# Kernel optimization log

Hardware: AMD Instinct MI355X
Metric: run time of the kernel (lower is better)

The kernel has to match this reference:

```python
import jax, jax.numpy as jnp
import numpy as np

B, S, D, H = 4, 1024, 256, 8  # batch, seq, d_model (== head_dim), n_heads
SCALE = 1.0 / float(np.sqrt(D))  # source references undefined self.scale; use 1/sqrt(d_model)


def setup_inputs() -> dict:
    key = jax.random.key(0)
    ks = jax.random.split(key, 11)
    w = 0.02
    return {
        "value_input": jax.random.normal(ks[0], (B, S, D), dtype=jnp.float32),
        "key_input": jax.random.normal(ks[1], (B, S, D), dtype=jnp.float32),
        "query_input": jax.random.normal(ks[2], (B, S, D), dtype=jnp.float32),
        "Wv": jax.random.normal(ks[3], (D, D * H), dtype=jnp.float32) * w,
        "bv": jnp.zeros((D * H,), dtype=jnp.float32),
        "Wk": jax.random.normal(ks[4], (D, D * H), dtype=jnp.float32) * w,
        "bk": jnp.zeros((D * H,), dtype=jnp.float32),
        "Wq": jax.random.normal(ks[5], (D, D * H), dtype=jnp.float32) * w,
        "bq": jnp.zeros((D * H,), dtype=jnp.float32),
        "Wo": jax.random.normal(ks[6], (D * H, D), dtype=jnp.float32) * w,
        "bo": jnp.zeros((D,), dtype=jnp.float32),
    }


def reference(value_input, key_input, query_input, Wv, bv, Wk, bk, Wq, bq, Wo, bo):
    # Fused QKV-style projections, then split into heads along last dim.
    # torch.split(..., d_model, dim=-1) == reshape to (B, S, H, D).
    v = (value_input @ Wv + bv).reshape(B, S, H, D)
    k = (key_input @ Wk + bk).reshape(B, S, H, D)
    q = (query_input @ Wq + bq).reshape(B, S, H, D)
    # Source: dot = k @ q^T  -> scores[b,h,key_pos,query_pos]
    scores = jnp.einsum('bkhd,bqhd->bhkq', k, q) * SCALE
    # Softmax over dim=-1 == the QUERY axis (faithful to source, nonstandard).
    attn = jax.nn.softmax(scores, axis=-1)
    # attn @ v : contract query axis with v's seq axis -> output indexed by key pos
    out_h = jnp.einsum('bhkq,bqhd->bkhd', attn, v)
    concat = out_h.reshape(B, S, H * D)
    return concat @ Wo + bo
```

## Files before the change

### kernel.cpp

```cpp
#include <hip/hip_runtime.h>
#include <cstddef>
#include <cstdint>

#define Bz 4
#define Sz 1024
#define Dm 256
#define Hh 8
#define DHh 2048
#define SCALE 0.0625f

typedef __attribute__((ext_vector_type(8))) short short8;
typedef __attribute__((ext_vector_type(16))) float f32x16;

__device__ inline unsigned short f2bf(float f){
  unsigned u = __float_as_uint(f);
  u += 0x7FFFu + ((u >> 16) & 1u);
  return (unsigned short)(u >> 16);
}
__device__ inline unsigned pk2(float a, float b){
  return (unsigned)f2bf(a) | ((unsigned)f2bf(b) << 16);
}
__device__ inline void gll16(const void* g, void* l){
  __builtin_amdgcn_global_load_lds((const __attribute__((address_space(1))) unsigned*)g,
                                   (__attribute__((address_space(3))) unsigned*)l, 16, 0, 0);
}
__device__ inline short8 lds8(const char* p){ return *(const short8*)p; }
__device__ inline f32x16 MM(short8 a, short8 b, f32x16 c){
  return __builtin_amdgcn_mfma_f32_32x32x16_bf16(a, b, c, 0, 0, 0);
}
__device__ inline f32x16 z16(){ f32x16 v;
#pragma unroll
  for(int i=0;i<16;i++) v[i]=0.f; return v; }

__global__ __launch_bounds__(256) void cvt_all(
    const float* __restrict__ S0, const float* __restrict__ S1, const float* __restrict__ S2,
    unsigned short* __restrict__ D0, unsigned short* __restrict__ D1, unsigned short* __restrict__ D2,
    const float* __restrict__ W0, const float* __restrict__ W1,
    const float* __restrict__ W2, const float* __restrict__ W3,
    unsigned short* __restrict__ T0, unsigned short* __restrict__ T1,
    unsigned short* __restrict__ T2, unsigned short* __restrict__ T3){
  __shared__ float t[32][33];
  int bx = blockIdx.x;
  if(bx < 3072){
    const int seg = bx >> 10;
    const float* src = seg==0 ? S0 : seg==1 ? S1 : S2;
    unsigned short* dst = seg==0 ? D0 : seg==1 ? D1 : D2;
    const int i = (bx & 1023)*256 + threadIdx.x;
    float4 v = ((const float4*)src)[i];
    ushort4 o; o.x=f2bf(v.x); o.y=f2bf(v.y); o.z=f2bf(v.z); o.w=f2bf(v.w);
    ((ushort4*)dst)[i] = o;
    return;
  }
  bx -= 3072;
  const int z = bx >> 9, inner = bx & 511;
  const float* W = z==0 ? W0 : z==1 ? W1 : z==2 ? W2 : W3;
  unsigned short* T = z==0 ? T0 : z==1 ? T1 : z==2 ? T2 : T3;
  const int K = (z<3) ? 256 : 2048;
  const int N = (z<3) ? 2048 : 256;
  const int n0 = (z<3) ? (inner & 63)*32 : (inner & 7)*32;
  const int k0 = (z<3) ? (inner >> 6)*32 : (inner >> 3)*32;
  const int a = threadIdx.x >> 5, c = threadIdx.x & 31;
#pragma unroll
  for(int p=0;p<4;p++)
    t[a + p*8][c] = W[(size_t)(k0 + a + p*8)*N + n0 + c];
  __syncthreads();
#pragma unroll
  for(int p=0;p<4;p++)
    T[(size_t)(n0 + a + p*8)*K + k0 + c] = f2bf(t[c][a + p*8]);
}

__global__ __launch_bounds__(256) void gemm_proj_all(
    const unsigned short* __restrict__ A0, const unsigned short* __restrict__ A1,
    const unsigned short* __restrict__ A2,
    const unsigned short* __restrict__ B0, const unsigned short* __restrict__ B1,
    const unsigned short* __restrict__ B2,
    const float* __restrict__ bias0, const float* __restrict__ bias1,
    const float* __restrict__ bias2,
    unsigned short* __restrict__ C0, unsigned short* __restrict__ C1,
    unsigned short* __restrict__ C2){
  __shared__ __align__(16) char sm[65536];
  const int z = blockIdx.z;
  const unsigned short* A = z==0 ? A0 : z==1 ? A1 : A2;
  const unsigned short* Bt = z==0 ? B0 : z==1 ? B1 : B2;
  const float* bias = z==0 ? bias0 : z==1 ? bias1 : bias2;
  unsigned short* C = z==0 ? C0 : z==1 ? C1 : C2;
  const int tid = threadIdx.x, w = tid>>6, lane = tid&63, l31 = lane&31, hp = lane>>5;
  const int wm = (w>>1)*64, wn = (w&1)*64;
  const int bm = blockIdx.y*128, bn = blockIdx.x*128;
  f32x16 acc[2][2]; acc[0][0]=z16(); acc[0][1]=z16(); acc[1][0]=z16(); acc[1][1]=z16();

  auto STAGE = [&](int db, int kk){
#pragma unroll
    for(int j=0;j<4;j++){
      int ci = (w*4+j)*64 + lane;
      int m = ci>>3, sl = ci&7;
      gll16(A  + (size_t)(bm+m)*256 + kk + ((sl ^ (m&7))<<3), sm + db*32768 + (w*4+j)*1024);
      gll16(Bt + (size_t)(bn+m)*256 + kk + ((sl ^ (m&7))<<3), sm + db*32768 + 16384 + (w*4+j)*1024);
    }
  };

  STAGE(0, 0);
  __syncthreads();
  int db = 0;
  for(int t=0; t<4; ++t){
    if(t<3) STAGE(db^1, (t+1)*64);
    const char* base = sm + db*32768;
#pragma unroll
    for(int s=0;s<4;s++){
      int m0 = wm + l31, m1 = wm + 32 + l31;
      int n0 = wn + l31, n1 = wn + 32 + l31;
      short8 a0 = lds8(base + m0*128 + (((s*2+hp) ^ (m0&7))<<4));
      short8 a1 = lds8(base + m1*128 + (((s*2+hp) ^ (m1&7))<<4));
      short8 b0 = lds8(base + 16384 + n0*128 + (((s*2+hp) ^ (n0&7))<<4));
      short8 b1 = lds8(base + 16384 + n1*128 + (((s*2+hp) ^ (n1&7))<<4));
      acc[0][0] = MM(a0,b0,acc[0][0]); acc[0][1] = MM(a0,b1,acc[0][1]);
      acc[1][0] = MM(a1,b0,acc[1][0]); acc[1][1] = MM(a1,b1,acc[1][1]);
    }
    __syncthreads();
    db ^= 1;
  }
#pragma unroll
  for(int nh=0; nh<2; nh++){
    int ncol = bn + wn + nh*32 + l31;
    float bb = bias[ncol];
#pragma unroll
    for(int mh=0; mh<2; mh++){
      if(z == 0){
        int hidx = ncol >> 8, d = ncol & 255;
#pragma unroll
        for(int gq=0; gq<4; gq++){
          int mrow = bm + wm + mh*32 + 8*gq + 4*hp;
          int batch = mrow >> 10, sin = mrow & 1023;
          unsigned u0 = pk2(acc[mh][nh][4*gq+0] + bb, acc[mh][nh][4*gq+1] + bb);
          unsigned u1 = pk2(acc[mh][nh][4*gq+2] + bb, acc[mh][nh][4*gq+3] + bb);
          uint2 uu; uu.x = u0; uu.y = u1;
          *(uint2*)(C + ((size_t)((batch*Hh + hidx)*Dm + d))*Sz + sin) = uu;
        }
      } else {
        float sc = (z == 1) ? SCALE : 1.0f;
#pragma unroll
        for(int r=0; r<16; r++){
          int mrow = bm + wm + mh*32 + (r&3) + 8*(r>>2) + 4*hp;
          C[(size_t)mrow*DHh + ncol] = f2bf((acc[mh][nh][r] + bb) * sc);
        }
      }
    }
  }
}

__global__ __launch_bounds__(256, 2) void attn_mfma(
    const unsigned short* __restrict__ Kp, const unsigned short* __restrict__ Qp,
    const unsigned short* __restrict__ Vt, unsigned short* __restrict__ Oc){
  __shared__ __align__(16) char sm[66560];
  const int tid = threadIdx.x, w = tid>>6, lane = tid&63, l31 = lane&31, hp = lane>>5;
  const int rg = w&1, set = w>>1;
  const int bid = blockIdx.x;
  const int xcd = bid & 7, inner = bid >> 3;
  const int rb = inner & 15, gsub = inner >> 4;
  const int g = gsub*8 + xcd, b = g >> 3, h = g & 7;
  const int brow0 = rb * 64;
  const size_t vtbase = ((size_t)((b*Hh + h)*Dm))*Sz;

  short8 kp[16];
  {
    const unsigned short* kr = Kp + (size_t)(b*Sz + brow0 + rg*32 + l31)*DHh + h*Dm + hp*8;
#pragma unroll
    for(int ki=0; ki<16; ki++) kp[ki] = *(const short8*)(kr + ki*16);
  }
  f32x16 acc[8];
#pragma unroll
  for(int f=0; f<8; f++) acc[f] = z16();
  float m_run = -3.0e38f, l_run = 0.f;
  char* qpL = sm + set*16384;
  char* vtL = sm + 32768 + set*16384;

  auto STAGE = [&](int it){
    const int kv0 = set*512 + it*32;
#pragma unroll
    for(int j=0; j<8; j++){
      int slot = j*2 + rg;
      int ci = slot*64 + lane;
      int c = ci>>5, sl5 = ci&31;
      gll16(Qp + (size_t)(b*Sz + kv0 + c)*DHh + h*Dm + ((sl5 ^ c)<<3),
            qpL + slot*1024);
      int dp = ci>>3, sv = (ci&7) ^ (dp&7);
      int d = dp*2 + (sv>>2), co = (sv&3)*8;
      gll16(Vt + vtbase + (size_t)d*Sz + kv0 + co, vtL + slot*1024);
    }
  };

  STAGE(0);
  __syncthreads();
  for(int it=0; it<16; ++it){
    f32x16 S = z16();
#pragma unroll
    for(int ki=0; ki<16; ki++){
      short8 a = lds8(qpL + l31*512 + (((ki*2+hp) ^ l31)<<4));
      S = MM(a, kp[ki], S);
    }
    float tmax = S[0];
#pragma unroll
    for(int r=1; r<16; r++) tmax = fmaxf(tmax, S[r]);
    tmax = fmaxf(tmax, __shfl_xor(tmax, 32));
    if(!__all(tmax <= m_run + 8.0f)){
      float mnew = fmaxf(m_run, tmax);
      float alpha = __expf(m_run - mnew);
      m_run = mnew; l_run *= alpha;
#pragma unroll
      for(int r=0; r<16; r++){
        int rr = (r&3) + 8*(r>>2) + 4*hp;
        float ar = __shfl(alpha, rr);
#pragma unroll
        for(int f=0; f<8; f++) acc[f][r] *= ar;
      }
    }
    float lsum = 0.f;
#pragma unroll
    for(int r=0; r<16; r++){ S[r] = __expf(S[r] - m_run); lsum += S[r]; }
    lsum += __shfl_xor(lsum, 32);
    l_run += lsum;
    short8 pa[2];
#pragma unroll
    for(int t=0; t<2; t++){
      unsigned w01 = pk2(S[t*8+0], S[t*8+1]);
      unsigned w23 = pk2(S[t*8+2], S[t*8+3]);
      unsigned w45 = pk2(S[t*8+4], S[t*8+5]);
      unsigned w67 = pk2(S[t*8+6], S[t*8+7]);
      unsigned x01 = __shfl_xor(w01, 32), x23 = __shfl_xor(w23, 32);
      unsigned x45 = __shfl_xor(w45, 32), x67 = __shfl_xor(w67, 32);
      union { unsigned u[4]; short8 s8; } U;
      if(hp == 0){ U.u[0]=w01; U.u[1]=w23; U.u[2]=x01; U.u[3]=x23; }
      else       { U.u[0]=x45; U.u[1]=x67; U.u[2]=w45; U.u[3]=w67; }
      pa[t] = U.s8;
    }
#pragma unroll
    for(int t=0; t<2; t++){
#pragma unroll
      for(int f=0; f<8; f++){
        int d = f*32 + l31;
        int dp = d>>1;
        int slot = (d&1)*4 + t*2 + hp;
        short8 vfr = lds8(vtL + dp*128 + ((slot ^ (dp&7))<<4));
        acc[f] = MM(pa[t], vfr, acc[f]);
      }
    }
    if(it < 15){
      __syncthreads();
      STAGE(it+1);
      __syncthreads();
    }
  }
  __syncthreads();
  float* stats = (float*)(sm + 65536);
  if(lane < 32){ stats[(w*32 + lane)*2 + 0] = m_run; stats[(w*32 + lane)*2 + 1] = l_run; }
  __syncthreads();
  float* mg = (float*)sm + rg*8192;
  if(set == 1){
    float mA = stats[(rg*32 + l31)*2 + 0];
    float mf = fmaxf(mA, m_run);
    float bB = __expf(m_run - mf);
#pragma unroll
    for(int r=0; r<16; r++){
      int rr = (r&3) + 8*(r>>2) + 4*hp;
      float br = __shfl(bB, rr);
#pragma unroll
      for(int f=0; f<8; f++) mg[rr*256 + f*32 + l31] = acc[f][r]*br;
    }
  }
  __syncthreads();
  if(set == 0){
    float mB = stats[((2+rg)*32 + l31)*2 + 0];
    float lB = stats[((2+rg)*32 + l31)*2 + 1];
    float mf = fmaxf(m_run, mB);
    float bA = __expf(m_run - mf), bBv = __expf(mB - mf);
    float inv = 1.0f / (l_run*bA + lB*bBv);
#pragma unroll
    for(int r=0; r<16; r++){
      int rr = (r&3) + 8*(r>>2) + 4*hp;
      float bAr = __shfl(bA, rr);
      float invr = __shfl(inv, rr);
      int srow = brow0 + rg*32 + rr;
#pragma unroll
      for(int f=0; f<8; f++){
        float v = (acc[f][r]*bAr + mg[rr*256 + f*32 + l31]) * invr;
        Oc[(size_t)(b*Sz + srow)*DHh + h*Dm + f*32 + l31] = f2bf(v);
      }
    }
  }
}

__global__ __launch_bounds__(256) void gemm_out(const unsigned short* __restrict__ A,
    const unsigned short* __restrict__ Bt, const float* __restrict__ bias,
    float* __restrict__ C){
  __shared__ __align__(16) char sm[32768];
  const int tid = threadIdx.x, w = tid>>6, lane = tid&63, l31 = lane&31, hp = lane>>5;
  const int wm = (w>>1)*32, wn = (w&1)*32;
  const int bm = blockIdx.y*64, bn = blockIdx.x*64;
  f32x16 acc = z16();

  auto STAGE = [&](int db, int kk){
#pragma unroll
    for(int j=0; j<2; j++){
      int ci = (w*2+j)*64 + lane;
      int m = ci>>3, sl = ci&7;
      gll16(A  + (size_t)(bm+m)*DHh + kk + ((sl ^ (m&7))<<3), sm + db*16384 + (w*2+j)*1024);
      gll16(Bt + (size_t)(bn+m)*DHh + kk + ((sl ^ (m&7))<<3), sm + db*16384 + 8192 + (w*2+j)*1024);
    }
  };

  STAGE(0, 0);
  __syncthreads();
  int db = 0;
  for(int t=0; t<32; ++t){
    if(t<31) STAGE(db^1, (t+1)*64);
    const char* base = sm + db*16384;
#pragma unroll
    for(int s=0; s<4; s++){
      int m0 = wm + l31, n0 = wn + l31;
      short8 a = lds8(base + m0*128 + (((s*2+hp) ^ (m0&7))<<4));
      short8 b = lds8(base + 8192 + n0*128 + (((s*2+hp) ^ (n0&7))<<4));
      acc = MM(a, b, acc);
    }
    __syncthreads();
    db ^= 1;
  }
  float bb = bias[bn + wn + l31];
#pragma unroll
  for(int r=0; r<16; r++){
    int mrow = bm + wm + (r&3) + 8*(r>>2) + 4*hp;
    C[(size_t)mrow*Dm + bn + wn + l31] = acc[r] + bb;
  }
}

extern "C" void kernel_launch(void* const* d_in, const int* in_sizes, int n_in,
                              void* d_out, int out_size, void* d_ws, size_t ws_size,
                              hipStream_t stream){
  (void)in_sizes; (void)n_in; (void)out_size; (void)ws_size;
  const float* value_in = (const float*)d_in[0];
  const float* key_in   = (const float*)d_in[1];
  const float* query_in = (const float*)d_in[2];
  const float* Wv = (const float*)d_in[3];
  const float* bv = (const float*)d_in[4];
  const float* Wk = (const float*)d_in[5];
  const float* bk = (const float*)d_in[6];
  const float* Wq = (const float*)d_in[7];
  const float* bq = (const float*)d_in[8];
  const float* Wo = (const float*)d_in[9];
  const float* bo = (const float*)d_in[10];

  char* ws = (char*)d_ws;
  unsigned short* av  = (unsigned short*)(ws + ((size_t) 0u<<20));
  unsigned short* ak  = (unsigned short*)(ws + ((size_t) 2u<<20));
  unsigned short* aq  = (unsigned short*)(ws + ((size_t) 4u<<20));
  unsigned short* wtv = (unsigned short*)(ws + ((size_t) 6u<<20));
  unsigned short* wtk = (unsigned short*)(ws + ((size_t) 7u<<20));
  unsigned short* wtq = (unsigned short*)(ws + ((size_t) 8u<<20));
  unsigned short* wto = (unsigned short*)(ws + ((size_t) 9u<<20));
  unsigned short* vt  = (unsigned short*)(ws + ((size_t)10u<<20));
  unsigned short* kb  = (unsigned short*)(ws + ((size_t)26u<<20));
  unsigned short* qb  = (unsigned short*)(ws + ((size_t)42u<<20));
  unsigned short* cc  = (unsigned short*)(ws + ((size_t)58u<<20));

  cvt_all<<<5120, 256, 0, stream>>>(value_in, key_in, query_in, av, ak, aq,
                                    Wv, Wk, Wq, Wo, wtv, wtk, wtq, wto);

  gemm_proj_all<<<dim3(16, 32, 3), 256, 0, stream>>>(
      av, ak, aq, wtv, wtk, wtq, bv, bk, bq, vt, kb, qb);

  attn_mfma<<<512, 256, 0, stream>>>(kb, qb, vt, cc);

  gemm_out<<<dim3(4, 64), 256, 0, stream>>>(cc, wto, bo, (float*)d_out);
}
```

Before: 253.3 us.

## Restructure attention: 512-thread blocks, double-buffered Q, V read from global in fragment layout

The V projection output is written in a blocked layout (seq blocks of 8 × d × 8), so the attention kernel can load V fragments straight from global memory into registers instead of staging them through LDS. Only Q is staged, now double-buffered so the next tile's load overlaps the current compute, which removes one barrier per iteration. Blocks grow to 512 threads covering 128 rows with a new block-to-head mapping, and MFMA sections are wrapped in s_setprio. The cost is more global-load traffic and latency on V, plus higher register pressure under the new launch bounds.

```diff
diff --git a/kernel.cpp b/kernel.cpp
--- a/kernel.cpp
+++ b/kernel.cpp
@@ -131,10 +131,11 @@
         for(int gq=0; gq<4; gq++){
           int mrow = bm + wm + mh*32 + 8*gq + 4*hp;
           int batch = mrow >> 10, sin = mrow & 1023;
+          int sblk = sin >> 3;
           unsigned u0 = pk2(acc[mh][nh][4*gq+0] + bb, acc[mh][nh][4*gq+1] + bb);
           unsigned u1 = pk2(acc[mh][nh][4*gq+2] + bb, acc[mh][nh][4*gq+3] + bb);
           uint2 uu; uu.x = u0; uu.y = u1;
-          *(uint2*)(C + ((size_t)((batch*Hh + hidx)*Dm + d))*Sz + sin) = uu;
+          *(uint2*)(C + ((size_t)((batch*Hh + hidx)*128 + sblk)*256 + d)*8 + 4*hp) = uu;
         }
       } else {
         float sc = (z == 1) ? SCALE : 1.0f;
@@ -148,22 +149,21 @@
   }
 }
 
-__global__ __launch_bounds__(256, 2) void attn_mfma(
+__global__ __launch_bounds__(512, 2) void attn_mfma(
     const unsigned short* __restrict__ Kp, const unsigned short* __restrict__ Qp,
     const unsigned short* __restrict__ Vt, unsigned short* __restrict__ Oc){
-  __shared__ __align__(16) char sm[66560];
+  __shared__ __align__(16) char sm[67584];
   const int tid = threadIdx.x, w = tid>>6, lane = tid&63, l31 = lane&31, hp = lane>>5;
-  const int rg = w&1, set = w>>1;
+  const int set = w>>2, ws = w&3;
   const int bid = blockIdx.x;
-  const int xcd = bid & 7, inner = bid >> 3;
-  const int rb = inner & 15, gsub = inner >> 4;
-  const int g = gsub*8 + xcd, b = g >> 3, h = g & 7;
-  const int brow0 = rb * 64;
-  const size_t vtbase = ((size_t)((b*Hh + h)*Dm))*Sz;
+  const int g = (bid & 7)*4 + (bid >> 6);
+  const int b = g >> 3, h = g & 7;
+  const int brow0 = ((bid >> 3) & 7) * 128;
+  const size_t vtbase = (size_t)(b*Hh + h) * (Sz*Dm);
 
   short8 kp[16];
   {
-    const unsigned short* kr = Kp + (size_t)(b*Sz + brow0 + rg*32 + l31)*DHh + h*Dm + hp*8;
+    const unsigned short* kr = Kp + (size_t)(b*Sz + brow0 + ws*32 + l31)*DHh + h*Dm + hp*8;
 #pragma unroll
     for(int ki=0; ki<16; ki++) kp[ki] = *(const short8*)(kr + ki*16);
   }
@@ -171,33 +171,34 @@
 #pragma unroll
   for(int f=0; f<8; f++) acc[f] = z16();
   float m_run = -3.0e38f, l_run = 0.f;
-  char* qpL = sm + set*16384;
-  char* vtL = sm + 32768 + set*16384;
-
-  auto STAGE = [&](int it){
+
+  auto STAGE = [&](int db, int it){
     const int kv0 = set*512 + it*32;
-#pragma unroll
-    for(int j=0; j<8; j++){
-      int slot = j*2 + rg;
+    char* qpD = sm + db*32768 + set*16384;
+#pragma unroll
+    for(int j=0; j<4; j++){
+      int slot = ws*4 + j;
       int ci = slot*64 + lane;
       int c = ci>>5, sl5 = ci&31;
       gll16(Qp + (size_t)(b*Sz + kv0 + c)*DHh + h*Dm + ((sl5 ^ c)<<3),
-            qpL + slot*1024);
-      int dp = ci>>3, sv = (ci&7) ^ (dp&7);
-      int d = dp*2 + (sv>>2), co = (sv&3)*8;
-      gll16(Vt + vtbase + (size_t)d*Sz + kv0 + co, vtL + slot*1024);
+            qpD + slot*1024);
     }
   };
 
-  STAGE(0);
-  __syncthreads();
+  STAGE(0, 0);
+  __syncthreads();
+  int db = 0;
   for(int it=0; it<16; ++it){
+    if(it<15) STAGE(db^1, it+1);
+    const char* qpL = sm + db*32768 + set*16384;
     f32x16 S = z16();
+    __builtin_amdgcn_s_setprio(1);
 #pragma unroll
     for(int ki=0; ki<16; ki++){
       short8 a = lds8(qpL + l31*512 + (((ki*2+hp) ^ l31)<<4));
       S = MM(a, kp[ki], S);
     }
+    __builtin_amdgcn_s_setprio(0);
     float tmax = S[0];
 #pragma unroll
     for(int r=1; r<16; r++) tmax = fmaxf(tmax, S[r]);
@@ -233,57 +234,60 @@
       else       { U.u[0]=x45; U.u[1]=x67; U.u[2]=w45; U.u[3]=w67; }
       pa[t] = U.s8;
     }
+    const int sb0 = set*64 + it*4;
 #pragma unroll
     for(int t=0; t<2; t++){
-#pragma unroll
-      for(int f=0; f<8; f++){
-        int d = f*32 + l31;
-        int dp = d>>1;
-        int slot = (d&1)*4 + t*2 + hp;
-        short8 vfr = lds8(vtL + dp*128 + ((slot ^ (dp&7))<<4));
-        acc[f] = MM(pa[t], vfr, acc[f]);
-      }
-    }
-    if(it < 15){
-      __syncthreads();
-      STAGE(it+1);
-      __syncthreads();
-    }
+      const unsigned short* vrow = Vt + vtbase + (size_t)(sb0 + t*2 + hp)*2048;
+      short8 vf[8];
+#pragma unroll
+      for(int f=0; f<8; f++)
+        vf[f] = *(const short8*)(vrow + (f*32 + l31)*8);
+      __builtin_amdgcn_s_setprio(1);
+#pragma unroll
+      for(int f=0; f<8; f++) acc[f] = MM(pa[t], vf[f], acc[f]);
+      __builtin_amdgcn_s_setprio(0);
+    }
+    __syncthreads();
+    db ^= 1;
   }
   __syncthreads();
   float* stats = (float*)(sm + 65536);
   if(lane < 32){ stats[(w*32 + lane)*2 + 0] = m_run; stats[(w*32 + lane)*2 + 1] = l_run; }
-  __syncthreads();
-  float* mg = (float*)sm + rg*8192;
-  if(set == 1){
-    float mA = stats[(rg*32 + l31)*2 + 0];
-    float mf = fmaxf(mA, m_run);
-    float bB = __expf(m_run - mf);
-#pragma unroll
-    for(int r=0; r<16; r++){
-      int rr = (r&3) + 8*(r>>2) + 4*hp;
-      float br = __shfl(bB, rr);
-#pragma unroll
-      for(int f=0; f<8; f++) mg[rr*256 + f*32 + l31] = acc[f][r]*br;
-    }
-  }
-  __syncthreads();
-  if(set == 0){
-    float mB = stats[((2+rg)*32 + l31)*2 + 0];
-    float lB = stats[((2+rg)*32 + l31)*2 + 1];
-    float mf = fmaxf(m_run, mB);
-    float bA = __expf(m_run - mf), bBv = __expf(mB - mf);
-    float inv = 1.0f / (l_run*bA + lB*bBv);
-#pragma unroll
-    for(int r=0; r<16; r++){
-      int rr = (r&3) + 8*(r>>2) + 4*hp;
-      float bAr = __shfl(bA, rr);
-      float invr = __shfl(inv, rr);
-      int srow = brow0 + rg*32 + rr;
-#pragma unroll
-      for(int f=0; f<8; f++){
-        float v = (acc[f][r]*bAr + mg[rr*256 + f*32 + l31]) * invr;
-        Oc[(size_t)(b*Sz + srow)*DHh + h*Dm + f*32 + l31] = f2bf(v);
+#pragma unroll
+  for(int p=0; p<2; p++){
+    __syncthreads();
+    if(set == 1 && (ws>>1) == p){
+      float mA = stats[(ws*32 + l31)*2 + 0];
+      float mf = fmaxf(mA, m_run);
+      float bB = __expf(m_run - mf);
+      float* mg = (float*)sm + (ws&1)*8192;
+#pragma unroll
+      for(int r=0; r<16; r++){
+        int rr = (r&3) + 8*(r>>2) + 4*hp;
+        float br = __shfl(bB, rr);
+#pragma unroll
+        for(int f=0; f<8; f++) mg[rr*256 + f*32 + l31] = acc[f][r]*br;
+      }
+    }
+    __syncthreads();
+    if(set == 0 && (ws>>1) == p){
+      float mB = stats[((4+ws)*32 + l31)*2 + 0];
+      float lB = stats[((4+ws)*32 + l31)*2 + 1];
+      float mf = fmaxf(m_run, mB);
+      float bA = __expf(m_run - mf), bBv = __expf(mB - mf);
+      float inv = 1.0f / (l_run*bA + lB*bBv);
+      float* mg = (float*)sm + (ws&1)*8192;
+#pragma unroll
+      for(int r=0; r<16; r++){
+        int rr = (r&3) + 8*(r>>2) + 4*hp;
+        float bAr = __shfl(bA, rr);
+        float invr = __shfl(inv, rr);
+        int srow = brow0 + ws*32 + rr;
+#pragma unroll
+        for(int f=0; f<8; f++){
+          float v = (acc[f][r]*bAr + mg[rr*256 + f*32 + l31]) * invr;
+          Oc[(size_t)(b*Sz + srow)*DHh + h*Dm + f*32 + l31] = f2bf(v);
+        }
       }
     }
   }
@@ -367,7 +371,7 @@
   gemm_proj_all<<<dim3(16, 32, 3), 256, 0, stream>>>(
       av, ak, aq, wtv, wtk, wtq, bv, bk, bq, vt, kb, qb);
 
-  attn_mfma<<<512, 256, 0, stream>>>(kb, qb, vt, cc);
+  attn_mfma<<<256, 512, 0, stream>>>(kb, qb, vt, cc);
 
   gemm_out<<<dim3(4, 64), 256, 0, stream>>>(cc, wto, bo, (float*)d_out);
 }
```

Result: faster. 209.8 us (-17.2%).
